# Kernel tuning notes

Measured on AMD Instinct MI355X. Metric: run time of the kernel, lower is better.

## Reference

```python
import jax, jax.numpy as jnp
import numpy as np

DIM = 1024
HEADS = 16
HEAD_DIM = DIM // HEADS


def _alibi_slopes(n_heads):
    # standard geometric ALiBi slopes
    start = 2.0 ** (-8.0 / n_heads)
    return start ** np.arange(1, n_heads + 1)


def setup_inputs() -> dict:
    key = jax.random.key(0)
    k1, k2, k3 = jax.random.split(key, 3)
    B, T = 2, 2048
    x = jax.random.normal(k1, (B, T, DIM), dtype=jnp.float32)
    # ALiBi bias: slope_h * -(i - j) for j <= i (full matrix here, causal mask applied separately)
    pos = np.arange(T)
    rel = pos[None, :] - pos[:, None]  # (T, T), j - i
    slopes = _alibi_slopes(HEADS)  # (H,)
    alibi_bias = jnp.asarray(slopes[:, None, None] * rel[None, :, :], dtype=jnp.float32)  # (H, T, T)
    # xavier_uniform for weights, zeros for biases
    lim_qkv = float(np.sqrt(6.0 / (DIM + 3 * DIM)))
    Wqkv = jax.random.uniform(k2, (3 * DIM, DIM), minval=-lim_qkv, maxval=lim_qkv, dtype=jnp.float32)
    bqkv = jnp.zeros((3 * DIM,), dtype=jnp.float32)
    lim_out = float(np.sqrt(6.0 / (DIM + DIM)))
    Wout = jax.random.uniform(k3, (DIM, DIM), minval=-lim_out, maxval=lim_out, dtype=jnp.float32)
    bout = jnp.zeros((DIM,), dtype=jnp.float32)
    return {"x": x, "causal": 1, "alibi_bias": alibi_bias,
            "Wqkv": Wqkv, "bqkv": bqkv, "Wout": Wout, "bout": bout}


def reference(x, causal, alibi_bias, Wqkv, bqkv, Wout, bout):
    B, T, D = x.shape
    H, hd = HEADS, HEAD_DIM
    qkv = x @ Wqkv.T + bqkv  # (B, T, 3D)
    q, k, v = jnp.split(qkv, 3, axis=-1)
    def split_heads(t):
        return t.reshape(B, T, H, hd).transpose(0, 2, 1, 3)  # (B, H, T, hd)
    q, k, v = split_heads(q), split_heads(k), split_heads(v)
    scale = 1.0 / jnp.sqrt(jnp.asarray(hd, dtype=q.dtype))
    scores = jnp.einsum('bhqd,bhkd->bhqk', q, k) * scale  # (B, H, T, T)
    bias = alibi_bias[None]  # (1, H, T, T)
    if causal:
        cm = jnp.triu(jnp.ones((T, T), dtype=bool), k=1)
        bias = bias + jnp.where(cm, -jnp.inf, 0.0).astype(q.dtype)
    attn = jax.nn.softmax(scores + bias, axis=-1)
    y = jnp.einsum('bhqk,bhkd->bhqd', attn, v)  # (B, H, T, hd)
    y = y.transpose(0, 2, 1, 3).reshape(B, T, D)
    return y @ Wout.T + bout
```

## Files before the change

kernel.cpp:

```cpp
#include <hip/hip_runtime.h>
#include <cstddef>
#include <cstdint>

#define SEQ    2048
#define DMODEL 1024
#define NH     16
#define HD     64
#define NB     2

typedef __attribute__((ext_vector_type(8))) short short8;
typedef __attribute__((ext_vector_type(4))) float floatx4;

#define MFMA16(a, b, c) __builtin_amdgcn_mfma_f32_16x16x32_bf16((a), (b), (c), 0, 0, 0)

#define ASYNC16(gsrc, ldst) \
    __builtin_amdgcn_global_load_lds((const __attribute__((address_space(1))) void*)(gsrc), \
                                     (__attribute__((address_space(3))) void*)(ldst), 16, 0, 0)

__device__ __forceinline__ short f2bf(float f) {
    union { float f; unsigned u; } a; a.f = f;
    unsigned u = a.u;
    unsigned r = u + 0x7fffu + ((u >> 16) & 1u);
    return (short)(r >> 16);
}

#define NX4 1048576
#define NW4  786432
#define NO4  262144

__global__ __launch_bounds__(256)
void convert_kernel(const float* __restrict__ x, const float* __restrict__ wqkv,
                    const float* __restrict__ wout,
                    short* __restrict__ xb, short* __restrict__ wqkvb,
                    short* __restrict__ woutb)
{
    int i = blockIdx.x * 256 + threadIdx.x;
    const float* src; short* dst; int off;
    if (i < NX4)            { src = x;    dst = xb;    off = i; }
    else if (i < NX4 + NW4) { src = wqkv; dst = wqkvb; off = i - NX4; }
    else if (i < NX4 + NW4 + NO4) { src = wout; dst = woutb; off = i - NX4 - NW4; }
    else return;
    float4 f = ((const float4*)src)[off];
    short4 s;
    s.x = f2bf(f.x); s.y = f2bf(f.y); s.z = f2bf(f.z); s.w = f2bf(f.w);
    ((short4*)dst)[off] = s;
}


__device__ __forceinline__ void gemm_stage(const short* __restrict__ A,
                                           const short* __restrict__ W,
                                           short* As, short* Bs,
                                           int m0, int n0, int k0, int K, int tid)
{
#pragma unroll
    for (int l = 0; l < 4; ++l) {
        int c = l * 256 + tid;
        int row = c >> 3;
        int col8 = (c & 7) ^ (row & 7);
        ASYNC16(&A[(size_t)(m0 + row) * K + k0 + col8 * 8], &As[c * 8]);
        ASYNC16(&W[(size_t)(n0 + row) * K + k0 + col8 * 8], &Bs[c * 8]);
    }
}

__device__ __forceinline__ void gemm_core(const short* As, const short* Bs,
                                          floatx4 acc[4][4], int wm, int wn,
                                          int l15, int quad)
{
#pragma unroll
    for (int kc = 0; kc < 2; ++kc) {
        short8 a[4], b[4];
#pragma unroll
        for (int t = 0; t < 4; ++t) {
            int rowa = wm * 64 + t * 16 + l15;
            int rowb = wn * 64 + t * 16 + l15;
            int sw = (kc * 4 + quad) ^ (l15 & 7);
            a[t] = *(const short8*)&As[(rowa * 8 + sw) * 8];
            b[t] = *(const short8*)&Bs[(rowb * 8 + sw) * 8];
        }
#pragma unroll
        for (int i = 0; i < 4; ++i)
#pragma unroll
            for (int j = 0; j < 4; ++j)
                acc[i][j] = MFMA16(a[i], b[j], acc[i][j]);
    }
}

__global__ __launch_bounds__(256)
void gemm_qkv_bf16(const short* __restrict__ A, const short* __restrict__ W,
                   const float* __restrict__ bias,
                   short* __restrict__ qws, short* __restrict__ kws,
                   short* __restrict__ vtws)
{
    __shared__ short As[128 * 64];
    __shared__ short Bs[128 * 64];
    const int tid = threadIdx.x;
    const int wave = tid >> 6, lane = tid & 63;
    const int l15 = lane & 15, quad = lane >> 4;
    const int wm = wave >> 1, wn = wave & 1;
    const int m0 = blockIdx.y * 128, n0 = blockIdx.x * 128;

    floatx4 acc[4][4];
#pragma unroll
    for (int i = 0; i < 4; ++i)
#pragma unroll
        for (int j = 0; j < 4; ++j) acc[i][j] = (floatx4){0.f, 0.f, 0.f, 0.f};

    for (int k0 = 0; k0 < DMODEL; k0 += 64) {
        __syncthreads();
        gemm_stage(A, W, As, Bs, m0, n0, k0, DMODEL, tid);
        __syncthreads();
        gemm_core(As, Bs, acc, wm, wn, l15, quad);
    }

#pragma unroll
    for (int i = 0; i < 4; ++i) {
#pragma unroll
        for (int j = 0; j < 4; ++j) {
            int ntile = n0 + wn * 64 + j * 16;
            int n = ntile + l15;
            int which = n >> 10;
            int rr = n & 1023;
            int h = rr >> 6, d = rr & 63;
            float bv = bias[n];
#pragma unroll
            for (int r = 0; r < 4; ++r) {
                int m = m0 + wm * 64 + i * 16 + quad * 4 + r;
                int bb = m >> 11, t = m & 2047;
                short val = f2bf(acc[i][j][r] + bv);
                size_t hb = (size_t)(bb * NH + h);
                if (which == 0)      qws[(hb * SEQ + t) * HD + d] = val;
                else if (which == 1) kws[(hb * SEQ + t) * HD + d] = val;
                else                 vtws[(hb * HD + d) * SEQ + t] = val;
            }
        }
    }
}

__global__ __launch_bounds__(256)
void gemm_out_bf16(const short* __restrict__ A, const short* __restrict__ W,
                   const float* __restrict__ bias, float* __restrict__ out)
{
    __shared__ short As[128 * 64];
    __shared__ short Bs[128 * 64];
    const int tid = threadIdx.x;
    const int wave = tid >> 6, lane = tid & 63;
    const int l15 = lane & 15, quad = lane >> 4;
    const int wm = wave >> 1, wn = wave & 1;
    const int m0 = blockIdx.y * 128, n0 = blockIdx.x * 128;

    floatx4 acc[4][4];
#pragma unroll
    for (int i = 0; i < 4; ++i)
#pragma unroll
        for (int j = 0; j < 4; ++j) acc[i][j] = (floatx4){0.f, 0.f, 0.f, 0.f};

    for (int k0 = 0; k0 < DMODEL; k0 += 64) {
        __syncthreads();
        gemm_stage(A, W, As, Bs, m0, n0, k0, DMODEL, tid);
        __syncthreads();
        gemm_core(As, Bs, acc, wm, wn, l15, quad);
    }

#pragma unroll
    for (int i = 0; i < 4; ++i) {
#pragma unroll
        for (int j = 0; j < 4; ++j) {
            int n = n0 + wn * 64 + j * 16 + l15;
            float bv = bias[n];
#pragma unroll
            for (int r = 0; r < 4; ++r) {
                int m = m0 + wm * 64 + i * 16 + quad * 4 + r;
                out[(size_t)m * DMODEL + n] = acc[i][j][r] + bv;
            }
        }
    }
}


__global__ __launch_bounds__(256)
void attn_mfma(const short* __restrict__ q, const short* __restrict__ k,
               const short* __restrict__ vt, const int* __restrict__ causal_p,
               short* __restrict__ y)
{
    const int qt = blockIdx.x, h = blockIdx.y, b = blockIdx.z;
    const int tid = threadIdx.x;
    const int wave = tid >> 6, lane = tid & 63;
    const int l15 = lane & 15, quad = lane >> 4;
    const int q0 = qt * 64;
    const int causal = causal_p[0];
    const float slope = exp2f(-0.5f * (float)(h + 1));

    __shared__ short Ks[64 * 64];
    __shared__ short Vs[64 * 64];
    __shared__ short Ps[4][16 * 64];

    const size_t base = ((size_t)(b * NH + h)) * SEQ * HD;
    const size_t vbase = base;

    short8 aq[2];
    {
        int qrow = q0 + wave * 16 + l15;
#pragma unroll
        for (int kc = 0; kc < 2; ++kc)
            aq[kc] = *(const short8*)&q[base + (size_t)qrow * HD + kc * 32 + quad * 8];
    }

    float m_i[4], l_i[4];
    floatx4 o[4];
#pragma unroll
    for (int r = 0; r < 4; ++r) { m_i[r] = -1e30f; l_i[r] = 0.f; }
#pragma unroll
    for (int dt = 0; dt < 4; ++dt) o[dt] = (floatx4){0.f, 0.f, 0.f, 0.f};

    const int ktmax = causal ? qt : (SEQ / 64 - 1);
    for (int kt = 0; kt <= ktmax; ++kt) {
        const int k0 = kt * 64;
        __syncthreads();
#pragma unroll
        for (int l = 0; l < 2; ++l) {
            int c = l * 256 + tid;
            int row = c >> 3;
            int col8 = (c & 7) ^ (row & 7);
            ASYNC16(&k[base + (size_t)(k0 + row) * HD + col8 * 8], &Ks[c * 8]);
            ASYNC16(&vt[vbase + (size_t)row * SEQ + k0 + col8 * 8], &Vs[c * 8]);
        }
        __syncthreads();

        floatx4 s[4];
#pragma unroll
        for (int ct = 0; ct < 4; ++ct) {
            int rowb = ct * 16 + l15;
            int sw0 = (quad) ^ (l15 & 7);
            int sw1 = (4 + quad) ^ (l15 & 7);
            short8 bk0 = *(const short8*)&Ks[(rowb * 8 + sw0) * 8];
            short8 bk1 = *(const short8*)&Ks[(rowb * 8 + sw1) * 8];
            floatx4 z = (floatx4){0.f, 0.f, 0.f, 0.f};
            z = MFMA16(aq[0], bk0, z);
            z = MFMA16(aq[1], bk1, z);
            s[ct] = z;
        }

        const int gi_base = q0 + wave * 16 + quad * 4;
        float mnew[4];
#pragma unroll
        for (int r = 0; r < 4; ++r) {
            int gi = gi_base + r;
            float mx = -1e30f;
#pragma unroll
            for (int ct = 0; ct < 4; ++ct) {
                int gj = k0 + ct * 16 + l15;
                float sv = s[ct][r] * 0.125f + slope * (float)(gj - gi);
                if (causal && gj > gi) sv = -1e30f;
                s[ct][r] = sv;
                mx = fmaxf(mx, sv);
            }
            mnew[r] = mx;
        }
#pragma unroll
        for (int off = 1; off < 16; off <<= 1)
#pragma unroll
            for (int r = 0; r < 4; ++r)
                mnew[r] = fmaxf(mnew[r], __shfl_xor(mnew[r], off, 64));

        float alpha[4], ls[4];
#pragma unroll
        for (int r = 0; r < 4; ++r) {
            float mn = fmaxf(m_i[r], mnew[r]);
            alpha[r] = __expf(m_i[r] - mn);
            m_i[r] = mn;
            ls[r] = 0.f;
#pragma unroll
            for (int ct = 0; ct < 4; ++ct) {
                float p = __expf(s[ct][r] - mn);
                s[ct][r] = p;
                ls[r] += p;
            }
        }
#pragma unroll
        for (int off = 1; off < 16; off <<= 1)
#pragma unroll
            for (int r = 0; r < 4; ++r)
                ls[r] += __shfl_xor(ls[r], off, 64);
#pragma unroll
        for (int r = 0; r < 4; ++r) l_i[r] = l_i[r] * alpha[r] + ls[r];

        short* Pw = &Ps[wave][0];
#pragma unroll
        for (int ct = 0; ct < 4; ++ct) {
#pragma unroll
            for (int r = 0; r < 4; ++r) {
                int row = quad * 4 + r;
                int col = ct * 16 + l15;
                Pw[(row * 8 + ((col >> 3) ^ (row & 7))) * 8 + (col & 7)] = f2bf(s[ct][r]);
            }
        }
        asm volatile("s_waitcnt lgkmcnt(0)" ::: "memory");

        int swp0 = (quad) ^ (l15 & 7);
        int swp1 = (4 + quad) ^ (l15 & 7);
        short8 ap0 = *(const short8*)&Pw[(l15 * 8 + swp0) * 8];
        short8 ap1 = *(const short8*)&Pw[(l15 * 8 + swp1) * 8];

#pragma unroll
        for (int dt = 0; dt < 4; ++dt) {
            int rowv = dt * 16 + l15;
            short8 bv0 = *(const short8*)&Vs[(rowv * 8 + swp0) * 8];
            short8 bv1 = *(const short8*)&Vs[(rowv * 8 + swp1) * 8];
            floatx4 oo = o[dt];
#pragma unroll
            for (int r = 0; r < 4; ++r) oo[r] *= alpha[r];
            oo = MFMA16(ap0, bv0, oo);
            oo = MFMA16(ap1, bv1, oo);
            o[dt] = oo;
        }
    }

#pragma unroll
    for (int dt = 0; dt < 4; ++dt) {
#pragma unroll
        for (int r = 0; r < 4; ++r) {
            int row = q0 + wave * 16 + quad * 4 + r;
            int col = h * HD + dt * 16 + l15;
            y[(size_t)(b * SEQ + row) * DMODEL + col] = f2bf(o[dt][r] / l_i[r]);
        }
    }
}


extern "C" void kernel_launch(void* const* d_in, const int* in_sizes, int n_in,
                              void* d_out, int out_size, void* d_ws, size_t ws_size,
                              hipStream_t stream)
{
    const float* x    = (const float*)d_in[0];
    const int*   caus = (const int*)d_in[1];
    const float* Wqkv = (const float*)d_in[3];
    const float* bqkv = (const float*)d_in[4];
    const float* Wout = (const float*)d_in[5];
    const float* bout = (const float*)d_in[6];
    float* out = (float*)d_out;

    char* ws = (char*)d_ws;
    short* xb    = (short*)(ws);
    short* wqkvb = (short*)(ws + (8u  << 20));
    short* woutb = (short*)(ws + (14u << 20));
    short* qws   = (short*)(ws + (16u << 20));
    short* kws   = (short*)(ws + (24u << 20));
    short* vtws  = (short*)(ws + (32u << 20));
    short* yb    = (short*)(ws + (40u << 20));

    convert_kernel<<<8192, 256, 0, stream>>>(x, Wqkv, Wout, xb, wqkvb, woutb);

    dim3 g1(3072 / 128, 4096 / 128);
    gemm_qkv_bf16<<<g1, 256, 0, stream>>>(xb, wqkvb, bqkv, qws, kws, vtws);

    dim3 ga(SEQ / 64, NH, NB);
    attn_mfma<<<ga, 256, 0, stream>>>(qws, kws, vtws, caus, yb);

    dim3 g2(1024 / 128, 4096 / 128);
    gemm_out_bf16<<<g2, 256, 0, stream>>>(yb, woutb, bout, out);
}
```

Baseline: 525.9 us.

## Process 128 query rows per attention block and fold scale and ALiBi row term

The attention kernel now gives each wave two 16-row query tiles, so a block covers 128 queries and reuses each loaded K/V tile twice. V fragments are hoisted into registers once per key tile. The 1/8 scale moves into the QKV GEMM epilogue, and the ALiBi row term is folded into the running max so only a column term is added per score. The causal mask is now skipped for tiles that lie fully below the diagonal. The grid gets half as many blocks, which cuts parallelism on a causal workload that is already imbalanced, and register pressure rises.

```diff
diff --git a/kernel.cpp b/kernel.cpp
--- a/kernel.cpp
+++ b/kernel.cpp
@@ -116,8 +116,7 @@
     for (int i = 0; i < 4; ++i) {
 #pragma unroll
         for (int j = 0; j < 4; ++j) {
-            int ntile = n0 + wn * 64 + j * 16;
-            int n = ntile + l15;
+            int n = n0 + wn * 64 + j * 16 + l15;
             int which = n >> 10;
             int rr = n & 1023;
             int h = rr >> 6, d = rr & 63;
@@ -126,7 +125,9 @@
             for (int r = 0; r < 4; ++r) {
                 int m = m0 + wm * 64 + i * 16 + quad * 4 + r;
                 int bb = m >> 11, t = m & 2047;
-                short val = f2bf(acc[i][j][r] + bv);
+                float vv = acc[i][j][r] + bv;
+                if (which == 0) vv *= 0.125f;
+                short val = f2bf(vv);
                 size_t hb = (size_t)(bb * NH + h);
                 if (which == 0)      qws[(hb * SEQ + t) * HD + d] = val;
                 else if (which == 1) kws[(hb * SEQ + t) * HD + d] = val;
@@ -186,33 +187,41 @@
     const int tid = threadIdx.x;
     const int wave = tid >> 6, lane = tid & 63;
     const int l15 = lane & 15, quad = lane >> 4;
-    const int q0 = qt * 64;
+    const int q0 = qt * 128;
     const int causal = causal_p[0];
     const float slope = exp2f(-0.5f * (float)(h + 1));
 
     __shared__ short Ks[64 * 64];
     __shared__ short Vs[64 * 64];
-    __shared__ short Ps[4][16 * 64];
+    __shared__ short Ps[4][32 * 64];
 
     const size_t base = ((size_t)(b * NH + h)) * SEQ * HD;
-    const size_t vbase = base;
-
-    short8 aq[2];
-    {
-        int qrow = q0 + wave * 16 + l15;
+
+    short8 aq[2][2];
+#pragma unroll
+    for (int rt = 0; rt < 2; ++rt) {
+        int qrow = q0 + wave * 32 + rt * 16 + l15;
 #pragma unroll
         for (int kc = 0; kc < 2; ++kc)
-            aq[kc] = *(const short8*)&q[base + (size_t)qrow * HD + kc * 32 + quad * 8];
-    }
-
-    float m_i[4], l_i[4];
-    floatx4 o[4];
-#pragma unroll
-    for (int r = 0; r < 4; ++r) { m_i[r] = -1e30f; l_i[r] = 0.f; }
-#pragma unroll
-    for (int dt = 0; dt < 4; ++dt) o[dt] = (floatx4){0.f, 0.f, 0.f, 0.f};
-
-    const int ktmax = causal ? qt : (SEQ / 64 - 1);
+            aq[rt][kc] = *(const short8*)&q[base + (size_t)qrow * HD + kc * 32 + quad * 8];
+    }
+
+    float m_i[2][4], l_i[2][4];
+    floatx4 o[2][4];
+#pragma unroll
+    for (int rt = 0; rt < 2; ++rt)
+#pragma unroll
+        for (int r = 0; r < 4; ++r) { m_i[rt][r] = -1e30f; l_i[rt][r] = 0.f; }
+#pragma unroll
+    for (int rt = 0; rt < 2; ++rt)
+#pragma unroll
+        for (int dt = 0; dt < 4; ++dt) o[rt][dt] = (floatx4){0.f, 0.f, 0.f, 0.f};
+
+    const int sw0 = quad ^ (l15 & 7);
+    const int sw1 = (4 + quad) ^ (l15 & 7);
+    short* Pw = &Ps[wave][0];
+
+    const int ktmax = causal ? (2 * qt + 1) : (SEQ / 64 - 1);
     for (int kt = 0; kt <= ktmax; ++kt) {
         const int k0 = kt * 64;
         __syncthreads();
@@ -222,106 +231,127 @@
             int row = c >> 3;
             int col8 = (c & 7) ^ (row & 7);
             ASYNC16(&k[base + (size_t)(k0 + row) * HD + col8 * 8], &Ks[c * 8]);
-            ASYNC16(&vt[vbase + (size_t)row * SEQ + k0 + col8 * 8], &Vs[c * 8]);
-        }
-        __syncthreads();
-
-        floatx4 s[4];
-#pragma unroll
-        for (int ct = 0; ct < 4; ++ct) {
-            int rowb = ct * 16 + l15;
-            int sw0 = (quad) ^ (l15 & 7);
-            int sw1 = (4 + quad) ^ (l15 & 7);
-            short8 bk0 = *(const short8*)&Ks[(rowb * 8 + sw0) * 8];
-            short8 bk1 = *(const short8*)&Ks[(rowb * 8 + sw1) * 8];
-            floatx4 z = (floatx4){0.f, 0.f, 0.f, 0.f};
-            z = MFMA16(aq[0], bk0, z);
-            z = MFMA16(aq[1], bk1, z);
-            s[ct] = z;
-        }
-
-        const int gi_base = q0 + wave * 16 + quad * 4;
-        float mnew[4];
-#pragma unroll
-        for (int r = 0; r < 4; ++r) {
-            int gi = gi_base + r;
-            float mx = -1e30f;
-#pragma unroll
-            for (int ct = 0; ct < 4; ++ct) {
-                int gj = k0 + ct * 16 + l15;
-                float sv = s[ct][r] * 0.125f + slope * (float)(gj - gi);
-                if (causal && gj > gi) sv = -1e30f;
-                s[ct][r] = sv;
-                mx = fmaxf(mx, sv);
-            }
-            mnew[r] = mx;
-        }
-#pragma unroll
-        for (int off = 1; off < 16; off <<= 1)
-#pragma unroll
-            for (int r = 0; r < 4; ++r)
-                mnew[r] = fmaxf(mnew[r], __shfl_xor(mnew[r], off, 64));
-
-        float alpha[4], ls[4];
-#pragma unroll
-        for (int r = 0; r < 4; ++r) {
-            float mn = fmaxf(m_i[r], mnew[r]);
-            alpha[r] = __expf(m_i[r] - mn);
-            m_i[r] = mn;
-            ls[r] = 0.f;
-#pragma unroll
-            for (int ct = 0; ct < 4; ++ct) {
-                float p = __expf(s[ct][r] - mn);
-                s[ct][r] = p;
-                ls[r] += p;
-            }
-        }
-#pragma unroll
-        for (int off = 1; off < 16; off <<= 1)
-#pragma unroll
-            for (int r = 0; r < 4; ++r)
-                ls[r] += __shfl_xor(ls[r], off, 64);
-#pragma unroll
-        for (int r = 0; r < 4; ++r) l_i[r] = l_i[r] * alpha[r] + ls[r];
-
-        short* Pw = &Ps[wave][0];
-#pragma unroll
-        for (int ct = 0; ct < 4; ++ct) {
-#pragma unroll
-            for (int r = 0; r < 4; ++r) {
-                int row = quad * 4 + r;
-                int col = ct * 16 + l15;
-                Pw[(row * 8 + ((col >> 3) ^ (row & 7))) * 8 + (col & 7)] = f2bf(s[ct][r]);
-            }
-        }
-        asm volatile("s_waitcnt lgkmcnt(0)" ::: "memory");
-
-        int swp0 = (quad) ^ (l15 & 7);
-        int swp1 = (4 + quad) ^ (l15 & 7);
-        short8 ap0 = *(const short8*)&Pw[(l15 * 8 + swp0) * 8];
-        short8 ap1 = *(const short8*)&Pw[(l15 * 8 + swp1) * 8];
-
+            ASYNC16(&vt[base + (size_t)row * SEQ + k0 + col8 * 8], &Vs[c * 8]);
+        }
+        __syncthreads();
+
+        short8 bv0[4], bv1[4];
 #pragma unroll
         for (int dt = 0; dt < 4; ++dt) {
             int rowv = dt * 16 + l15;
-            short8 bv0 = *(const short8*)&Vs[(rowv * 8 + swp0) * 8];
-            short8 bv1 = *(const short8*)&Vs[(rowv * 8 + swp1) * 8];
-            floatx4 oo = o[dt];
-#pragma unroll
-            for (int r = 0; r < 4; ++r) oo[r] *= alpha[r];
-            oo = MFMA16(ap0, bv0, oo);
-            oo = MFMA16(ap1, bv1, oo);
-            o[dt] = oo;
-        }
-    }
-
-#pragma unroll
-    for (int dt = 0; dt < 4; ++dt) {
-#pragma unroll
-        for (int r = 0; r < 4; ++r) {
-            int row = q0 + wave * 16 + quad * 4 + r;
-            int col = h * HD + dt * 16 + l15;
-            y[(size_t)(b * SEQ + row) * DMODEL + col] = f2bf(o[dt][r] / l_i[r]);
+            bv0[dt] = *(const short8*)&Vs[(rowv * 8 + sw0) * 8];
+            bv1[dt] = *(const short8*)&Vs[(rowv * 8 + sw1) * 8];
+        }
+
+        float bj[4];
+#pragma unroll
+        for (int ct = 0; ct < 4; ++ct)
+            bj[ct] = slope * (float)(k0 + ct * 16 + l15);
+
+        float alpha[2][4];
+#pragma unroll
+        for (int rt = 0; rt < 2; ++rt) {
+            floatx4 s[4];
+#pragma unroll
+            for (int ct = 0; ct < 4; ++ct) {
+                int rowb = ct * 16 + l15;
+                short8 bk0 = *(const short8*)&Ks[(rowb * 8 + sw0) * 8];
+                short8 bk1 = *(const short8*)&Ks[(rowb * 8 + sw1) * 8];
+                floatx4 z = (floatx4){0.f, 0.f, 0.f, 0.f};
+                z = MFMA16(aq[rt][0], bk0, z);
+                z = MFMA16(aq[rt][1], bk1, z);
+                s[ct] = z;
+            }
+
+            const int gi_min = q0 + wave * 32 + rt * 16;
+            const int gi_base = gi_min + quad * 4;
+            const bool maskrt = causal && (k0 + 63 > gi_min);
+
+            float mx[4];
+#pragma unroll
+            for (int r = 0; r < 4; ++r) {
+                mx[r] = -1e30f;
+#pragma unroll
+                for (int ct = 0; ct < 4; ++ct) {
+                    float t = s[ct][r] + bj[ct];
+                    if (maskrt && (k0 + ct * 16 + l15 > gi_base + r)) t = -1e30f;
+                    s[ct][r] = t;
+                    mx[r] = fmaxf(mx[r], t);
+                }
+            }
+#pragma unroll
+            for (int off = 1; off < 16; off <<= 1)
+#pragma unroll
+                for (int r = 0; r < 4; ++r)
+                    mx[r] = fmaxf(mx[r], __shfl_xor(mx[r], off, 64));
+
+            float ls[4];
+#pragma unroll
+            for (int r = 0; r < 4; ++r) {
+                float sl_gi = slope * (float)(gi_base + r);
+                float mn = fmaxf(m_i[rt][r], mx[r] - sl_gi);
+                alpha[rt][r] = __expf(m_i[rt][r] - mn);
+                m_i[rt][r] = mn;
+                float cc = mn + sl_gi;
+                ls[r] = 0.f;
+#pragma unroll
+                for (int ct = 0; ct < 4; ++ct) {
+                    float p = __expf(s[ct][r] - cc);
+                    s[ct][r] = p;
+                    ls[r] += p;
+                }
+            }
+#pragma unroll
+            for (int off = 1; off < 16; off <<= 1)
+#pragma unroll
+                for (int r = 0; r < 4; ++r)
+                    ls[r] += __shfl_xor(ls[r], off, 64);
+#pragma unroll
+            for (int r = 0; r < 4; ++r)
+                l_i[rt][r] = l_i[rt][r] * alpha[rt][r] + ls[r];
+
+#pragma unroll
+            for (int ct = 0; ct < 4; ++ct) {
+#pragma unroll
+                for (int r = 0; r < 4; ++r) {
+                    int row = rt * 16 + quad * 4 + r;
+                    int col = ct * 16 + l15;
+                    Pw[(row * 8 + ((col >> 3) ^ (row & 7))) * 8 + (col & 7)] = f2bf(s[ct][r]);
+                }
+            }
+#pragma unroll
+            for (int dt = 0; dt < 4; ++dt)
+#pragma unroll
+                for (int r = 0; r < 4; ++r) o[rt][dt][r] *= alpha[rt][r];
+        }
+
+        __syncthreads();
+
+#pragma unroll
+        for (int rt = 0; rt < 2; ++rt) {
+            int prow = rt * 16 + l15;
+            short8 ap0 = *(const short8*)&Pw[(prow * 8 + sw0) * 8];
+            short8 ap1 = *(const short8*)&Pw[(prow * 8 + sw1) * 8];
+#pragma unroll
+            for (int dt = 0; dt < 4; ++dt) {
+                floatx4 oo = o[rt][dt];
+                oo = MFMA16(ap0, bv0[dt], oo);
+                oo = MFMA16(ap1, bv1[dt], oo);
+                o[rt][dt] = oo;
+            }
+        }
+    }
+
+#pragma unroll
+    for (int rt = 0; rt < 2; ++rt) {
+#pragma unroll
+        for (int dt = 0; dt < 4; ++dt) {
+#pragma unroll
+            for (int r = 0; r < 4; ++r) {
+                int row = q0 + wave * 32 + rt * 16 + quad * 4 + r;
+                int col = h * HD + dt * 16 + l15;
+                y[(size_t)(b * SEQ + row) * DMODEL + col] = f2bf(o[rt][dt][r] / l_i[rt][r]);
+            }
         }
     }
 }
@@ -353,9 +383,9 @@
     dim3 g1(3072 / 128, 4096 / 128);
     gemm_qkv_bf16<<<g1, 256, 0, stream>>>(xb, wqkvb, bqkv, qws, kws, vtws);
 
-    dim3 ga(SEQ / 64, NH, NB);
+    dim3 ga(SEQ / 128, NH, NB);
     attn_mfma<<<ga, 256, 0, stream>>>(qws, kws, vtws, caus, yb);
 
-    dim3 g2(1024 / 128, 4096 / 128);
+    dim3 g2(DMODEL / 128, 4096 / 128);
     gemm_out_bf16<<<g2, 256, 0, stream>>>(yb, woutb, bout, out);
 }
```

After: 538.4 us. +2.4%, slower.
